# Performance work log

Hardware: AMD Instinct MI355X
Metric: run time of the kernel (lower is better)

Reference implementation:

```python
import jax, jax.numpy as jnp
import numpy as np

B, S, D, H, E, P, TOP_K = 8, 4096, 512, 2048, 8, 16, 2


def setup_inputs() -> dict:
    key = jax.random.key(0)
    ks = jax.random.split(key, 7)
    x = jax.random.normal(ks[0], (B, S, D), dtype=jnp.float32)
    pattern_ids = jax.random.randint(ks[1], (B,), 0, P)
    # router params (init per module: std 0.01 content, std 0.1 pattern bias)
    Wr = 0.01 * jax.random.normal(ks[2], (D, E), dtype=jnp.float32)
    Wp = 0.1 * jax.random.normal(ks[3], (P, E), dtype=jnp.float32)
    # per-expert SwiGLU FFN weights (stacked): w1, w3: [E,D,H], w2: [E,H,D]
    W1 = jax.random.normal(ks[4], (E, D, H), dtype=jnp.float32) / np.float32(np.sqrt(D))
    W2 = jax.random.normal(ks[5], (E, H, D), dtype=jnp.float32) / np.float32(np.sqrt(H))
    W3 = jax.random.normal(ks[6], (E, D, H), dtype=jnp.float32) / np.float32(np.sqrt(D))
    return {"x": x, "pattern_ids": pattern_ids, "Wr": Wr, "Wp": Wp, "W1": W1, "W2": W2, "W3": W3}


def reference(x, pattern_ids, Wr, Wp, W1, W2, W3):
    num_experts = W1.shape[0]
    num_patterns = Wp.shape[0]
    # ---- pattern-aware router ----
    # content logits + per-batch pattern bias broadcast over seq
    logits = jnp.einsum('bsd,de->bse', x, Wr) + Wp[pattern_ids][:, None, :]  # [B,S,E]
    top_w, top_i = jax.lax.top_k(logits, TOP_K)           # [B,S,K]
    gates = jax.nn.softmax(top_w, axis=-1)                # softmax over the top-k logits
    # ---- expert dispatch / combine (loop over small fixed expert count) ----
    y = jnp.zeros_like(x)
    for e in range(num_experts):
        # combined gate weight for expert e per token (0 if not selected)
        w_e = jnp.sum(gates * (top_i == e), axis=-1)      # [B,S]
        h = jnp.einsum('bsd,dh->bsh', x, W1[e]) * jax.nn.silu(jnp.einsum('bsd,dh->bsh', x, W3[e]))
        y = y + w_e[..., None] * jnp.einsum('bsh,hd->bsd', h, W2[e])
    # ---- auxiliary losses ----
    probs = jax.nn.softmax(logits, axis=-1)
    router_z_loss = jnp.mean(jnp.square(logits)) * 0.001
    balance_loss = jnp.mean(jnp.square(probs.mean(axis=(0, 1)) - 1.0 / num_experts))
    Pn = jax.nn.softmax(Wp, axis=-1)
    sim = Pn @ Pn.T
    specialization_loss = jnp.mean(sim * (1.0 - jnp.eye(num_patterns, dtype=sim.dtype))) * 0.1
    return (y, router_z_loss, balance_loss, specialization_loss)
```

## Files before the change

kernel.cpp:

```cpp
#include <hip/hip_runtime.h>
#include <hip/hip_bf16.h>
#include <math.h>


#define B_ 8
#define S_ 4096
#define D_ 512
#define H_ 2048
#define E_ 8
#define P_ 16
#define NTOK (B_ * S_)
#define NPAIR (NTOK * 2)

typedef __bf16 bf16;
typedef __bf16 bf16x8 __attribute__((ext_vector_type(8)));
typedef float f32x4 __attribute__((ext_vector_type(4)));

#define OFF_GATES 256
#define OFF_LIST (OFF_GATES + NPAIR * 4)
#define OFF_XBF (OFF_LIST + E_ * NTOK * 4)
#define OFF_W13T (OFF_XBF + (size_t)NTOK * D_ * 2)
#define OFF_W2T (OFF_W13T + (size_t)E_ * 2 * H_ * D_ * 2)
#define OFF_HBUF (OFF_W2T + (size_t)E_ * D_ * H_ * 2)
#define WS_NEEDED (OFF_HBUF + (size_t)NTOK * H_ * 2)

__device__ __forceinline__ void gl16(const bf16* g, bf16* l) {
  __builtin_amdgcn_global_load_lds((const __attribute__((address_space(1))) unsigned int*)g,
                                   (__attribute__((address_space(3))) unsigned int*)l, 16, 0, 0);
}

__global__ __launch_bounds__(256) void router_kernel(
    const float* __restrict__ x, const int* __restrict__ pids,
    const float* __restrict__ Wr, const float* __restrict__ Wp,
    bf16* __restrict__ xbf, float* __restrict__ gates, int* __restrict__ lists,
    int* __restrict__ counts, float* __restrict__ probSum, float* __restrict__ zSum) {
  __shared__ float xs[32 * 516];
  __shared__ float wr_s[E_ * 516];
  __shared__ float wp_s[E_];
  __shared__ float probAcc[E_];
  __shared__ float zAcc;
  __shared__ int lcnt[E_], lbase[E_];
  __shared__ float lg_s[32][E_ + 1];

  const int tid = threadIdx.x;
  const int tok0 = blockIdx.x * 32;

#pragma unroll
  for (int rep = 0; rep < (D_ * E_) / 256; ++rep) {
    int flat = rep * 256 + tid;
    wr_s[(flat & 7) * 516 + (flat >> 3)] = Wr[flat];
  }
  if (tid < E_) {
    wp_s[tid] = Wp[pids[tok0 >> 12] * E_ + tid];
    probAcc[tid] = 0.f;
    lcnt[tid] = 0;
  }
  if (tid == 0) zAcc = 0.f;

  const float4* x4 = (const float4*)(x + (size_t)tok0 * D_);
#pragma unroll
  for (int rep = 0; rep < 16; ++rep) {
    int idx = rep * 256 + tid;
    float4 v = x4[idx];
    int t = idx >> 7;
    int d = (idx & 127) * 4;
    *(float4*)(xs + t * 516 + d) = v;
    union { unsigned short u[4]; uint2 qq; } pk;
    pk.u[0] = __builtin_bit_cast(unsigned short, (bf16)v.x);
    pk.u[1] = __builtin_bit_cast(unsigned short, (bf16)v.y);
    pk.u[2] = __builtin_bit_cast(unsigned short, (bf16)v.z);
    pk.u[3] = __builtin_bit_cast(unsigned short, (bf16)v.w);
    *(uint2*)(xbf + (size_t)tok0 * D_ + (size_t)idx * 4) = pk.qq;
  }
  __syncthreads();

  const int t = tid >> 3, e = tid & 7;
  const int lane = tid & 63;
  {
    float a0 = 0.f, a1 = 0.f, a2 = 0.f, a3 = 0.f;
    const float* xr = xs + t * 516;
    const float* wr = wr_s + e * 516;
#pragma unroll 8
    for (int d = 0; d < D_; d += 4) {
      float4 xv = *(const float4*)(xr + d);
      float4 wv = *(const float4*)(wr + d);
      a0 += xv.x * wv.x;
      a1 += xv.y * wv.y;
      a2 += xv.z * wv.z;
      a3 += xv.w * wv.w;
    }
    lg_s[t][e] = (a0 + a1) + (a2 + a3) + wp_s[e];
  }
  __syncthreads();

  float v[E_];
#pragma unroll
  for (int k = 0; k < E_; ++k) v[k] = lg_s[t][k];
  const float lg = v[e];
  float m = v[0];
#pragma unroll
  for (int k = 1; k < E_; ++k) m = fmaxf(m, v[k]);
  float s = 0.f;
#pragma unroll
  for (int k = 0; k < E_; ++k) s += expf(v[k] - m);
  float prob = expf(lg - m) / s;
  float z = lg * lg;
  int i1 = 0;
  float v1 = v[0];
#pragma unroll
  for (int k = 1; k < E_; ++k)
    if (v[k] > v1) { v1 = v[k]; i1 = k; }
  int i2 = -1;
  float v2 = -1e30f;
#pragma unroll
  for (int k = 0; k < E_; ++k)
    if (k != i1 && v[k] > v2) { v2 = v[k]; i2 = k; }

  float p = prob;
  p += __shfl_xor(p, 8);
  p += __shfl_xor(p, 16);
  p += __shfl_xor(p, 32);
  float zz = z;
#pragma unroll
  for (int off = 1; off < 64; off <<= 1) zz += __shfl_xor(zz, off);
  if (lane < 8) atomicAdd(&probAcc[e], p);
  if (lane == 0) atomicAdd(&zAcc, zz);

  int r = (e == i1) ? 0 : ((e == i2) ? 1 : -1);
  int pos = -1;
  if (r >= 0) {
    float ex = expf(v2 - v1);
    float g = (r == 0) ? 1.f / (1.f + ex) : ex / (1.f + ex);
    gates[(tok0 + t) * 2 + r] = g;
    pos = atomicAdd(&lcnt[e], 1);
  }
  __syncthreads();
  if (tid < E_) lbase[tid] = atomicAdd(&counts[tid], lcnt[tid]);
  __syncthreads();
  if (r >= 0) lists[e * NTOK + lbase[e] + pos] = (tok0 + t) * 2 + r;
  if (tid < E_) atomicAdd(&probSum[tid], probAcc[tid]);
  else if (tid == 8) atomicAdd(zSum, zAcc);
}

__global__ __launch_bounds__(256) void transpose_convert(const float* __restrict__ in,
                                                         bf16* __restrict__ out, int R, int C,
                                                         size_t out_estride, int mode) {
  const int e = blockIdx.z;
  const int r0 = blockIdx.y * 64, c0 = blockIdx.x * 64;
  in += (size_t)e * R * C;
  out += (size_t)e * out_estride;
  __shared__ unsigned int lt[64 * 33];

  const int tid = threadIdx.x;
  const int m = tid & 15, qq = tid >> 4;
#pragma unroll
  for (int rep = 0; rep < 2; ++rep) {
    int rp = qq + rep * 16;
    const float4 a = *(const float4*)(in + (size_t)(r0 + rp * 2) * C + c0 + m * 4);
    const float4 b = *(const float4*)(in + (size_t)(r0 + rp * 2 + 1) * C + c0 + m * 4);
#pragma unroll
    for (int j = 0; j < 4; ++j) {
      unsigned short lo = __builtin_bit_cast(unsigned short, (bf16)((&a.x)[j]));
      unsigned short hi = __builtin_bit_cast(unsigned short, (bf16)((&b.x)[j]));
      lt[(m * 4 + j) * 33 + rp] = (unsigned int)lo | ((unsigned int)hi << 16);
    }
  }
  __syncthreads();
  const int c = tid >> 2, dw0 = (tid & 3) * 8;
  unsigned int vv[8];
#pragma unroll
  for (int j = 0; j < 8; ++j) vv[j] = lt[c * 33 + dw0 + j];
  int orow = c0 + c;
  if (mode >= 0) orow = ((orow >> 4) << 5) | (orow & 15) | mode;
  uint4* dst = (uint4*)(out + (size_t)orow * R + r0 + dw0 * 2);
  dst[0] = make_uint4(vv[0], vv[1], vv[2], vv[3]);
  dst[1] = make_uint4(vv[4], vv[5], vv[6], vv[7]);
}

__global__ __launch_bounds__(256, 2) void gemm1_kernel(
    const bf16* __restrict__ xbf, const bf16* __restrict__ W13T,
    const int* __restrict__ counts, const int* __restrict__ lists,
    const float* __restrict__ gates, bf16* __restrict__ hbuf, int e) {
  const int count = counts[e];
  const int m0 = blockIdx.y * 128;
  if (m0 >= count) return;
  const int n0 = blockIdx.x * 128;
  const int* list_e = lists + e * NTOK;
  const bf16* Be = W13T + (size_t)e * (2 * H_) * D_;

  __shared__ bf16 sA[2 * 128 * 32];
  __shared__ bf16 sB[2 * 128 * 32];
  __shared__ int stok[128];
  __shared__ float sgate[128];

  const int tid = threadIdx.x;
  if (tid < 128) {
    int rg = m0 + tid;
    int pr = (rg < count) ? list_e[rg] : 0;
    stok[tid] = pr >> 1;
    sgate[tid] = (rg < count) ? gates[pr] : 0.f;
  }
  __syncthreads();

  const int wave = tid >> 6, lane = tid & 63;
  const int rsub = lane >> 2, kq = lane & 3;
  const int scol = (kq ^ ((lane >> 3) & 3)) * 8;
  const int rA0 = wave * 16 + rsub, rA1 = 64 + wave * 16 + rsub;
  const bf16* aP0 = xbf + (size_t)stok[rA0] * D_ + scol;
  const bf16* aP1 = xbf + (size_t)stok[rA1] * D_ + scol;
  const bf16* bP0 = Be + (size_t)(n0 + rA0) * D_ + scol;
  const bf16* bP1 = Be + (size_t)(n0 + rA1) * D_ + scol;
  bf16* lA0 = sA + wave * 512;
  bf16* lA1 = sA + (wave + 4) * 512;
  bf16* lB0 = sB + wave * 512;
  bf16* lB1 = sB + (wave + 4) * 512;

  const int wm = wave >> 1, wn = wave & 1;
  const int lm = lane & 15, q = lane >> 4;
  const int rq = (q ^ ((lm >> 1) & 3)) * 8;
  const bf16* aRd = sA + (wm * 64 + lm) * 32 + rq;
  const bf16* bRd = sB + (wn * 64 + lm) * 32 + rq;

  f32x4 acc[4][4] = {};

  gl16(aP0, lA0);
  gl16(aP1, lA1);
  gl16(bP0, lB0);
  gl16(bP1, lB1);
  __syncthreads();

  int cur = 0;
  for (int t = 1; t < D_ / 32; ++t) {
    const int koff = t * 32;
    const int nxt = (cur ^ 1) * 4096;
    gl16(aP0 + koff, lA0 + nxt);
    gl16(aP1 + koff, lA1 + nxt);
    gl16(bP0 + koff, lB0 + nxt);
    gl16(bP1 + koff, lB1 + nxt);
    const bf16* aR = aRd + cur * 4096;
    const bf16* bR = bRd + cur * 4096;
    bf16x8 af[4], bf_[4];
#pragma unroll
    for (int i = 0; i < 4; ++i) {
      af[i] = *(const bf16x8*)(aR + i * 512);
      bf_[i] = *(const bf16x8*)(bR + i * 512);
    }
#pragma unroll
    for (int mt = 0; mt < 4; ++mt)
#pragma unroll
      for (int nt = 0; nt < 4; ++nt)
        acc[mt][nt] =
            __builtin_amdgcn_mfma_f32_16x16x32_bf16(af[mt], bf_[nt], acc[mt][nt], 0, 0, 0);
    __syncthreads();
    cur ^= 1;
  }
  {
    const bf16* aR = aRd + cur * 4096;
    const bf16* bR = bRd + cur * 4096;
    bf16x8 af[4], bf_[4];
#pragma unroll
    for (int i = 0; i < 4; ++i) {
      af[i] = *(const bf16x8*)(aR + i * 512);
      bf_[i] = *(const bf16x8*)(bR + i * 512);
    }
#pragma unroll
    for (int mt = 0; mt < 4; ++mt)
#pragma unroll
      for (int nt = 0; nt < 4; ++nt)
        acc[mt][nt] =
            __builtin_amdgcn_mfma_f32_16x16x32_bf16(af[mt], bf_[nt], acc[mt][nt], 0, 0, 0);
  }

  const int hb = (n0 >> 1) + wn * 32;
#pragma unroll
  for (int mt = 0; mt < 4; ++mt) {
#pragma unroll
    for (int u = 0; u < 2; ++u) {
#pragma unroll
      for (int r = 0; r < 4; ++r) {
        int lrow = wm * 64 + mt * 16 + q * 4 + r;
        int grow = m0 + lrow;
        if (grow < count) {
          float v1 = acc[mt][2 * u][r];
          float v3 = acc[mt][2 * u + 1][r];
          float g = v1 * (v3 / (1.f + __expf(-v3))) * sgate[lrow];
          hbuf[(size_t)grow * H_ + hb + u * 16 + lm] = (bf16)g;
        }
      }
    }
  }
}

__global__ __launch_bounds__(256, 2) void gemm2_kernel(const bf16* __restrict__ hbuf,
                                                       const bf16* __restrict__ W2T,
                                                       const int* __restrict__ counts,
                                                       const int* __restrict__ lists,
                                                       float* __restrict__ y, int e) {
  const int count = counts[e];
  const int m0 = blockIdx.y * 128;
  if (m0 >= count) return;
  const int n0 = blockIdx.x * 128;
  const int kb = blockIdx.z * (H_ / 2);
  const bf16* W2e = W2T + (size_t)e * D_ * H_;
  const int* list_e = lists + e * NTOK;

  __shared__ bf16 sA[2 * 128 * 32];
  __shared__ bf16 sB[2 * 128 * 32];
  __shared__ int stok[128];

  const int tid = threadIdx.x;
  if (tid < 128) {
    int rg = m0 + tid;
    stok[tid] = (rg < count) ? (list_e[rg] >> 1) : 0;
  }
  __syncthreads();

  const int wave = tid >> 6, lane = tid & 63;
  const int rsub = lane >> 2, kq = lane & 3;
  const int scol = (kq ^ ((lane >> 3) & 3)) * 8;
  const int rA0 = wave * 16 + rsub, rA1 = 64 + wave * 16 + rsub;
  const bf16* aP0 = hbuf + (size_t)(m0 + rA0) * H_ + kb + scol;
  const bf16* aP1 = hbuf + (size_t)(m0 + rA1) * H_ + kb + scol;
  const bf16* bP0 = W2e + (size_t)(n0 + rA0) * H_ + kb + scol;
  const bf16* bP1 = W2e + (size_t)(n0 + rA1) * H_ + kb + scol;
  bf16* lA0 = sA + wave * 512;
  bf16* lA1 = sA + (wave + 4) * 512;
  bf16* lB0 = sB + wave * 512;
  bf16* lB1 = sB + (wave + 4) * 512;

  const int wm = wave >> 1, wn = wave & 1;
  const int lm = lane & 15, q = lane >> 4;
  const int rq = (q ^ ((lm >> 1) & 3)) * 8;
  const bf16* aRd = sA + (wm * 64 + lm) * 32 + rq;
  const bf16* bRd = sB + (wn * 64 + lm) * 32 + rq;

  f32x4 acc[4][4] = {};

  gl16(aP0, lA0);
  gl16(aP1, lA1);
  gl16(bP0, lB0);
  gl16(bP1, lB1);
  __syncthreads();

  int cur = 0;
  for (int t = 1; t < (H_ / 2) / 32; ++t) {
    const int koff = t * 32;
    const int nxt = (cur ^ 1) * 4096;
    gl16(aP0 + koff, lA0 + nxt);
    gl16(aP1 + koff, lA1 + nxt);
    gl16(bP0 + koff, lB0 + nxt);
    gl16(bP1 + koff, lB1 + nxt);
    const bf16* aR = aRd + cur * 4096;
    const bf16* bR = bRd + cur * 4096;
    bf16x8 af[4], bf_[4];
#pragma unroll
    for (int i = 0; i < 4; ++i) {
      af[i] = *(const bf16x8*)(aR + i * 512);
      bf_[i] = *(const bf16x8*)(bR + i * 512);
    }
#pragma unroll
    for (int mt = 0; mt < 4; ++mt)
#pragma unroll
      for (int nt = 0; nt < 4; ++nt)
        acc[mt][nt] =
            __builtin_amdgcn_mfma_f32_16x16x32_bf16(af[mt], bf_[nt], acc[mt][nt], 0, 0, 0);
    __syncthreads();
    cur ^= 1;
  }
  {
    const bf16* aR = aRd + cur * 4096;
    const bf16* bR = bRd + cur * 4096;
    bf16x8 af[4], bf_[4];
#pragma unroll
    for (int i = 0; i < 4; ++i) {
      af[i] = *(const bf16x8*)(aR + i * 512);
      bf_[i] = *(const bf16x8*)(bR + i * 512);
    }
#pragma unroll
    for (int mt = 0; mt < 4; ++mt)
#pragma unroll
      for (int nt = 0; nt < 4; ++nt)
        acc[mt][nt] =
            __builtin_amdgcn_mfma_f32_16x16x32_bf16(af[mt], bf_[nt], acc[mt][nt], 0, 0, 0);
  }

#pragma unroll
  for (int mt = 0; mt < 4; ++mt) {
#pragma unroll
    for (int nt = 0; nt < 4; ++nt) {
#pragma unroll
      for (int r = 0; r < 4; ++r) {
        int lrow = wm * 64 + mt * 16 + q * 4 + r;
        int grow = m0 + lrow;
        if (grow < count) {
          atomicAdd(&y[(size_t)stok[lrow] * D_ + n0 + wn * 64 + nt * 16 + lm], acc[mt][nt][r]);
        }
      }
    }
  }
}

__global__ __launch_bounds__(256) void finalize_kernel(const float* __restrict__ Wp,
                                                       const float* __restrict__ probSum,
                                                       const float* __restrict__ zSum,
                                                       float* __restrict__ out) {
  __shared__ float pn[P_][E_];
  __shared__ float simAcc;
  const int tid = threadIdx.x;
  if (tid == 0) simAcc = 0.f;
  if (tid < P_) {
    float v[E_], m = -1e30f, s = 0.f;
#pragma unroll
    for (int e = 0; e < E_; ++e) {
      v[e] = Wp[tid * E_ + e];
      m = fmaxf(m, v[e]);
    }
#pragma unroll
    for (int e = 0; e < E_; ++e) {
      float ex = expf(v[e] - m);
      pn[tid][e] = ex;
      s += ex;
    }
#pragma unroll
    for (int e = 0; e < E_; ++e) pn[tid][e] /= s;
  }
  __syncthreads();
  {
    int i = tid >> 4, j = tid & 15;
    if (i != j) {
      float d = 0.f;
#pragma unroll
      for (int e = 0; e < E_; ++e) d += pn[i][e] * pn[j][e];
      atomicAdd(&simAcc, d);
    }
  }
  __syncthreads();
  if (tid == 0) {
    out[0] = zSum[0] / (float)(NTOK * E_) * 0.001f;
    float bl = 0.f;
#pragma unroll
    for (int e = 0; e < E_; ++e) {
      float pm = probSum[e] / (float)NTOK - 1.f / (float)E_;
      bl += pm * pm;
    }
    out[1] = bl / (float)E_;
    out[2] = simAcc / (float)(P_ * P_) * 0.1f;
  }
}

extern "C" void kernel_launch(void* const* d_in, const int* in_sizes, int n_in, void* d_out,
                              int out_size, void* d_ws, size_t ws_size, hipStream_t stream) {
  const float* x = (const float*)d_in[0];
  const int* pids = (const int*)d_in[1];
  const float* Wr = (const float*)d_in[2];
  const float* Wp = (const float*)d_in[3];
  const float* W1 = (const float*)d_in[4];
  const float* W2 = (const float*)d_in[5];
  const float* W3 = (const float*)d_in[6];
  float* y = (float*)d_out;

  if (ws_size < WS_NEEDED) return;

  char* ws = (char*)d_ws;
  int* counts = (int*)ws;
  float* probSum = (float*)(ws + 32);
  float* zSum = (float*)(ws + 64);
  float* gates = (float*)(ws + OFF_GATES);
  int* lists = (int*)(ws + OFF_LIST);
  bf16* xbf = (bf16*)(ws + OFF_XBF);
  bf16* W13T = (bf16*)(ws + OFF_W13T);
  bf16* W2T = (bf16*)(ws + OFF_W2T);
  bf16* hbuf = (bf16*)(ws + OFF_HBUF);

  hipMemsetAsync(ws, 0, 256, stream);
  hipMemsetAsync(d_out, 0, (size_t)NTOK * D_ * 4, stream);

  router_kernel<<<dim3(NTOK / 32), 256, 0, stream>>>(x, pids, Wr, Wp, xbf, gates, lists, counts,
                                                     probSum, zSum);
  transpose_convert<<<dim3(H_ / 64, D_ / 64, E_), 256, 0, stream>>>(W1, W13T, D_, H_,
                                                                    (size_t)2 * H_ * D_, 0);
  transpose_convert<<<dim3(H_ / 64, D_ / 64, E_), 256, 0, stream>>>(W3, W13T, D_, H_,
                                                                    (size_t)2 * H_ * D_, 16);
  transpose_convert<<<dim3(D_ / 64, H_ / 64, E_), 256, 0, stream>>>(W2, W2T, H_, D_,
                                                                    (size_t)H_ * D_, -1);

  for (int e = 0; e < E_; ++e) {
    gemm1_kernel<<<dim3((2 * H_) / 128, NTOK / 128), 256, 0, stream>>>(xbf, W13T, counts, lists,
                                                                       gates, hbuf, e);
    gemm2_kernel<<<dim3(D_ / 128, NTOK / 128, 2), 256, 0, stream>>>(hbuf, W2T, counts, lists, y,
                                                                    e);
  }
  finalize_kernel<<<1, 256, 0, stream>>>(Wp, probSum, zSum, y + (size_t)NTOK * D_);
}
```

Before: 1.126 ms.

## Deepen GEMM global-to-LDS pipeline to four buffers with vmcnt-based waits

Both expert GEMM kernels move from a double-buffered LDS pipeline with a full __syncthreads per k-step to a four-slot ring that keeps two tiles in flight ahead of compute. Waits use explicit s_waitcnt vmcnt counts and a raw s_barrier, so compute can start while later loads are still outstanding. The goal is to hide global memory latency and remove full-drain barriers. In exchange, LDS use per block doubles, which may reduce occupancy, and correctness depends on the hand-counted vmcnt values and on the ring slots not being overwritten while another wave is still reading them.

```diff
diff --git a/kernel.cpp b/kernel.cpp
--- a/kernel.cpp
+++ b/kernel.cpp
@@ -188,8 +188,8 @@
   const int* list_e = lists + e * NTOK;
   const bf16* Be = W13T + (size_t)e * (2 * H_) * D_;
 
-  __shared__ bf16 sA[2 * 128 * 32];
-  __shared__ bf16 sB[2 * 128 * 32];
+  __shared__ bf16 sA[4 * 128 * 32];
+  __shared__ bf16 sB[4 * 128 * 32];
   __shared__ int stok[128];
   __shared__ float sgate[128];
 
@@ -210,10 +210,6 @@
   const bf16* aP1 = xbf + (size_t)stok[rA1] * D_ + scol;
   const bf16* bP0 = Be + (size_t)(n0 + rA0) * D_ + scol;
   const bf16* bP1 = Be + (size_t)(n0 + rA1) * D_ + scol;
-  bf16* lA0 = sA + wave * 512;
-  bf16* lA1 = sA + (wave + 4) * 512;
-  bf16* lB0 = sB + wave * 512;
-  bf16* lB1 = sB + (wave + 4) * 512;
 
   const int wm = wave >> 1, wn = wave & 1;
   const int lm = lane & 15, q = lane >> 4;
@@ -223,22 +219,18 @@
 
   f32x4 acc[4][4] = {};
 
-  gl16(aP0, lA0);
-  gl16(aP1, lA1);
-  gl16(bP0, lB0);
-  gl16(bP1, lB1);
-  __syncthreads();
-
-  int cur = 0;
-  for (int t = 1; t < D_ / 32; ++t) {
-    const int koff = t * 32;
-    const int nxt = (cur ^ 1) * 4096;
-    gl16(aP0 + koff, lA0 + nxt);
-    gl16(aP1 + koff, lA1 + nxt);
-    gl16(bP0 + koff, lB0 + nxt);
-    gl16(bP1 + koff, lB1 + nxt);
-    const bf16* aR = aRd + cur * 4096;
-    const bf16* bR = bRd + cur * 4096;
+  auto STAGE = [&](int t, int bi) {
+    const int ko = t * 32;
+    bf16* ba = sA + bi * 4096;
+    bf16* bb = sB + bi * 4096;
+    gl16(aP0 + ko, ba + wave * 512);
+    gl16(aP1 + ko, ba + (wave + 4) * 512);
+    gl16(bP0 + ko, bb + wave * 512);
+    gl16(bP1 + ko, bb + (wave + 4) * 512);
+  };
+  auto COMP = [&](int bi) {
+    const bf16* aR = aRd + bi * 4096;
+    const bf16* bR = bRd + bi * 4096;
     bf16x8 af[4], bf_[4];
 #pragma unroll
     for (int i = 0; i < 4; ++i) {
@@ -251,25 +243,22 @@
       for (int nt = 0; nt < 4; ++nt)
         acc[mt][nt] =
             __builtin_amdgcn_mfma_f32_16x16x32_bf16(af[mt], bf_[nt], acc[mt][nt], 0, 0, 0);
-    __syncthreads();
-    cur ^= 1;
-  }
-  {
-    const bf16* aR = aRd + cur * 4096;
-    const bf16* bR = bRd + cur * 4096;
-    bf16x8 af[4], bf_[4];
-#pragma unroll
-    for (int i = 0; i < 4; ++i) {
-      af[i] = *(const bf16x8*)(aR + i * 512);
-      bf_[i] = *(const bf16x8*)(bR + i * 512);
-    }
-#pragma unroll
-    for (int mt = 0; mt < 4; ++mt)
-#pragma unroll
-      for (int nt = 0; nt < 4; ++nt)
-        acc[mt][nt] =
-            __builtin_amdgcn_mfma_f32_16x16x32_bf16(af[mt], bf_[nt], acc[mt][nt], 0, 0, 0);
-  }
+  };
+
+  STAGE(0, 0);
+  STAGE(1, 1);
+  for (int t = 0; t < D_ / 32 - 2; ++t) {
+    STAGE(t + 2, (t + 2) & 3);
+    asm volatile("s_waitcnt vmcnt(8) lgkmcnt(0)" ::: "memory");
+    __builtin_amdgcn_s_barrier();
+    COMP(t & 3);
+  }
+  asm volatile("s_waitcnt vmcnt(4) lgkmcnt(0)" ::: "memory");
+  __builtin_amdgcn_s_barrier();
+  COMP((D_ / 32 - 2) & 3);
+  asm volatile("s_waitcnt vmcnt(0) lgkmcnt(0)" ::: "memory");
+  __builtin_amdgcn_s_barrier();
+  COMP((D_ / 32 - 1) & 3);
 
   const int hb = (n0 >> 1) + wn * 32;
 #pragma unroll
@@ -304,8 +293,8 @@
   const bf16* W2e = W2T + (size_t)e * D_ * H_;
   const int* list_e = lists + e * NTOK;
 
-  __shared__ bf16 sA[2 * 128 * 32];
-  __shared__ bf16 sB[2 * 128 * 32];
+  __shared__ bf16 sA[4 * 128 * 32];
+  __shared__ bf16 sB[4 * 128 * 32];
   __shared__ int stok[128];
 
   const int tid = threadIdx.x;
@@ -323,10 +312,6 @@
   const bf16* aP1 = hbuf + (size_t)(m0 + rA1) * H_ + kb + scol;
   const bf16* bP0 = W2e + (size_t)(n0 + rA0) * H_ + kb + scol;
   const bf16* bP1 = W2e + (size_t)(n0 + rA1) * H_ + kb + scol;
-  bf16* lA0 = sA + wave * 512;
-  bf16* lA1 = sA + (wave + 4) * 512;
-  bf16* lB0 = sB + wave * 512;
-  bf16* lB1 = sB + (wave + 4) * 512;
 
   const int wm = wave >> 1, wn = wave & 1;
   const int lm = lane & 15, q = lane >> 4;
@@ -336,22 +321,18 @@
 
   f32x4 acc[4][4] = {};
 
-  gl16(aP0, lA0);
-  gl16(aP1, lA1);
-  gl16(bP0, lB0);
-  gl16(bP1, lB1);
-  __syncthreads();
-
-  int cur = 0;
-  for (int t = 1; t < (H_ / 2) / 32; ++t) {
-    const int koff = t * 32;
-    const int nxt = (cur ^ 1) * 4096;
-    gl16(aP0 + koff, lA0 + nxt);
-    gl16(aP1 + koff, lA1 + nxt);
-    gl16(bP0 + koff, lB0 + nxt);
-    gl16(bP1 + koff, lB1 + nxt);
-    const bf16* aR = aRd + cur * 4096;
-    const bf16* bR = bRd + cur * 4096;
+  auto STAGE = [&](int t, int bi) {
+    const int ko = t * 32;
+    bf16* ba = sA + bi * 4096;
+    bf16* bb = sB + bi * 4096;
+    gl16(aP0 + ko, ba + wave * 512);
+    gl16(aP1 + ko, ba + (wave + 4) * 512);
+    gl16(bP0 + ko, bb + wave * 512);
+    gl16(bP1 + ko, bb + (wave + 4) * 512);
+  };
+  auto COMP = [&](int bi) {
+    const bf16* aR = aRd + bi * 4096;
+    const bf16* bR = bRd + bi * 4096;
     bf16x8 af[4], bf_[4];
 #pragma unroll
     for (int i = 0; i < 4; ++i) {
@@ -364,25 +345,23 @@
       for (int nt = 0; nt < 4; ++nt)
         acc[mt][nt] =
             __builtin_amdgcn_mfma_f32_16x16x32_bf16(af[mt], bf_[nt], acc[mt][nt], 0, 0, 0);
-    __syncthreads();
-    cur ^= 1;
-  }
-  {
-    const bf16* aR = aRd + cur * 4096;
-    const bf16* bR = bRd + cur * 4096;
-    bf16x8 af[4], bf_[4];
-#pragma unroll
-    for (int i = 0; i < 4; ++i) {
-      af[i] = *(const bf16x8*)(aR + i * 512);
-      bf_[i] = *(const bf16x8*)(bR + i * 512);
-    }
-#pragma unroll
-    for (int mt = 0; mt < 4; ++mt)
-#pragma unroll
-      for (int nt = 0; nt < 4; ++nt)
-        acc[mt][nt] =
-            __builtin_amdgcn_mfma_f32_16x16x32_bf16(af[mt], bf_[nt], acc[mt][nt], 0, 0, 0);
-  }
+  };
+
+  const int NT = (H_ / 2) / 32;
+  STAGE(0, 0);
+  STAGE(1, 1);
+  for (int t = 0; t < NT - 2; ++t) {
+    STAGE(t + 2, (t + 2) & 3);
+    asm volatile("s_waitcnt vmcnt(8) lgkmcnt(0)" ::: "memory");
+    __builtin_amdgcn_s_barrier();
+    COMP(t & 3);
+  }
+  asm volatile("s_waitcnt vmcnt(4) lgkmcnt(0)" ::: "memory");
+  __builtin_amdgcn_s_barrier();
+  COMP((NT - 2) & 3);
+  asm volatile("s_waitcnt vmcnt(0) lgkmcnt(0)" ::: "memory");
+  __builtin_amdgcn_s_barrier();
+  COMP((NT - 1) & 3);
 
 #pragma unroll
   for (int mt = 0; mt < 4; ++mt) {
```

Result: no change. 1.111 ms (-1.3%).

## Batch all experts into single grouped GEMM launches and deepen gemm2 pipeline

Applied to the files above, without the earlier changes.

Replaces the per-expert loop of 16 kernel launches with two launches that cover all experts via blockIdx.z, storing h rows for each expert at a prefix-sum offset in a larger hbuf. Experts can then run concurrently, removing launch gaps and the tail underutilization of each small per-expert grid. Separately, gemm2 moves from double buffering to a 4-stage LDS ring with explicit vmcnt waits, so loads are issued two steps ahead. This doubles gemm2's LDS use, and the fused path only runs when the workspace is large enough, falling back to the old loop otherwise.

```diff
diff --git a/kernel.cpp b/kernel.cpp
--- a/kernel.cpp
+++ b/kernel.cpp
@@ -23,6 +23,7 @@
 #define OFF_W2T (OFF_W13T + (size_t)E_ * 2 * H_ * D_ * 2)
 #define OFF_HBUF (OFF_W2T + (size_t)E_ * D_ * H_ * 2)
 #define WS_NEEDED (OFF_HBUF + (size_t)NTOK * H_ * 2)
+#define WS_FUSED (OFF_HBUF + (size_t)NPAIR * H_ * 2)
 
 __device__ __forceinline__ void gl16(const bf16* g, bf16* l) {
   __builtin_amdgcn_global_load_lds((const __attribute__((address_space(1))) unsigned int*)g,
@@ -180,10 +181,16 @@
 __global__ __launch_bounds__(256, 2) void gemm1_kernel(
     const bf16* __restrict__ xbf, const bf16* __restrict__ W13T,
     const int* __restrict__ counts, const int* __restrict__ lists,
-    const float* __restrict__ gates, bf16* __restrict__ hbuf, int e) {
+    const float* __restrict__ gates, bf16* __restrict__ hbuf, int e_param, int fuse) {
+  const int e = fuse ? (int)blockIdx.z : e_param;
   const int count = counts[e];
   const int m0 = blockIdx.y * 128;
   if (m0 >= count) return;
+  int hbase = 0;
+  if (fuse) {
+#pragma unroll
+    for (int j = 0; j < E_; ++j) hbase += (j < e) ? counts[j] : 0;
+  }
   const int n0 = blockIdx.x * 128;
   const int* list_e = lists + e * NTOK;
   const bf16* Be = W13T + (size_t)e * (2 * H_) * D_;
@@ -284,7 +291,7 @@
           float v1 = acc[mt][2 * u][r];
           float v3 = acc[mt][2 * u + 1][r];
           float g = v1 * (v3 / (1.f + __expf(-v3))) * sgate[lrow];
-          hbuf[(size_t)grow * H_ + hb + u * 16 + lm] = (bf16)g;
+          hbuf[(size_t)(hbase + grow) * H_ + hb + u * 16 + lm] = (bf16)g;
         }
       }
     }
@@ -295,17 +302,26 @@
                                                        const bf16* __restrict__ W2T,
                                                        const int* __restrict__ counts,
                                                        const int* __restrict__ lists,
-                                                       float* __restrict__ y, int e) {
+                                                       float* __restrict__ y, int e_param,
+                                                       int fuse) {
+  const int zz = (int)blockIdx.z;
+  const int e = fuse ? (zz >> 1) : e_param;
+  const int kc = fuse ? (zz & 1) : zz;
   const int count = counts[e];
   const int m0 = blockIdx.y * 128;
   if (m0 >= count) return;
+  int hbase = 0;
+  if (fuse) {
+#pragma unroll
+    for (int j = 0; j < E_; ++j) hbase += (j < e) ? counts[j] : 0;
+  }
   const int n0 = blockIdx.x * 128;
-  const int kb = blockIdx.z * (H_ / 2);
+  const int kb = kc * (H_ / 2);
   const bf16* W2e = W2T + (size_t)e * D_ * H_;
   const int* list_e = lists + e * NTOK;
 
-  __shared__ bf16 sA[2 * 128 * 32];
-  __shared__ bf16 sB[2 * 128 * 32];
+  __shared__ bf16 sA[4 * 128 * 32];
+  __shared__ bf16 sB[4 * 128 * 32];
   __shared__ int stok[128];
 
   const int tid = threadIdx.x;
@@ -319,14 +335,10 @@
   const int rsub = lane >> 2, kq = lane & 3;
   const int scol = (kq ^ ((lane >> 3) & 3)) * 8;
   const int rA0 = wave * 16 + rsub, rA1 = 64 + wave * 16 + rsub;
-  const bf16* aP0 = hbuf + (size_t)(m0 + rA0) * H_ + kb + scol;
-  const bf16* aP1 = hbuf + (size_t)(m0 + rA1) * H_ + kb + scol;
+  const bf16* aP0 = hbuf + (size_t)(hbase + m0 + rA0) * H_ + kb + scol;
+  const bf16* aP1 = hbuf + (size_t)(hbase + m0 + rA1) * H_ + kb + scol;
   const bf16* bP0 = W2e + (size_t)(n0 + rA0) * H_ + kb + scol;
   const bf16* bP1 = W2e + (size_t)(n0 + rA1) * H_ + kb + scol;
-  bf16* lA0 = sA + wave * 512;
-  bf16* lA1 = sA + (wave + 4) * 512;
-  bf16* lB0 = sB + wave * 512;
-  bf16* lB1 = sB + (wave + 4) * 512;
 
   const int wm = wave >> 1, wn = wave & 1;
   const int lm = lane & 15, q = lane >> 4;
@@ -336,22 +348,18 @@
 
   f32x4 acc[4][4] = {};
 
-  gl16(aP0, lA0);
-  gl16(aP1, lA1);
-  gl16(bP0, lB0);
-  gl16(bP1, lB1);
-  __syncthreads();
-
-  int cur = 0;
-  for (int t = 1; t < (H_ / 2) / 32; ++t) {
-    const int koff = t * 32;
-    const int nxt = (cur ^ 1) * 4096;
-    gl16(aP0 + koff, lA0 + nxt);
-    gl16(aP1 + koff, lA1 + nxt);
-    gl16(bP0 + koff, lB0 + nxt);
-    gl16(bP1 + koff, lB1 + nxt);
-    const bf16* aR = aRd + cur * 4096;
-    const bf16* bR = bRd + cur * 4096;
+  auto STAGE = [&](int t, int bi) {
+    const int ko = t * 32;
+    bf16* ba = sA + bi * 4096;
+    bf16* bb = sB + bi * 4096;
+    gl16(aP0 + ko, ba + wave * 512);
+    gl16(aP1 + ko, ba + (wave + 4) * 512);
+    gl16(bP0 + ko, bb + wave * 512);
+    gl16(bP1 + ko, bb + (wave + 4) * 512);
+  };
+  auto COMP = [&](int bi) {
+    const bf16* aR = aRd + bi * 4096;
+    const bf16* bR = bRd + bi * 4096;
     bf16x8 af[4], bf_[4];
 #pragma unroll
     for (int i = 0; i < 4; ++i) {
@@ -364,25 +372,23 @@
       for (int nt = 0; nt < 4; ++nt)
         acc[mt][nt] =
             __builtin_amdgcn_mfma_f32_16x16x32_bf16(af[mt], bf_[nt], acc[mt][nt], 0, 0, 0);
-    __syncthreads();
-    cur ^= 1;
-  }
-  {
-    const bf16* aR = aRd + cur * 4096;
-    const bf16* bR = bRd + cur * 4096;
-    bf16x8 af[4], bf_[4];
-#pragma unroll
-    for (int i = 0; i < 4; ++i) {
-      af[i] = *(const bf16x8*)(aR + i * 512);
-      bf_[i] = *(const bf16x8*)(bR + i * 512);
-    }
-#pragma unroll
-    for (int mt = 0; mt < 4; ++mt)
-#pragma unroll
-      for (int nt = 0; nt < 4; ++nt)
-        acc[mt][nt] =
-            __builtin_amdgcn_mfma_f32_16x16x32_bf16(af[mt], bf_[nt], acc[mt][nt], 0, 0, 0);
-  }
+  };
+
+  const int NT = (H_ / 2) / 32;
+  STAGE(0, 0);
+  STAGE(1, 1);
+  for (int t = 0; t < NT - 2; ++t) {
+    STAGE(t + 2, (t + 2) & 3);
+    asm volatile("s_waitcnt vmcnt(8) lgkmcnt(0)" ::: "memory");
+    __builtin_amdgcn_s_barrier();
+    COMP(t & 3);
+  }
+  asm volatile("s_waitcnt vmcnt(4) lgkmcnt(0)" ::: "memory");
+  __builtin_amdgcn_s_barrier();
+  COMP((NT - 2) & 3);
+  asm volatile("s_waitcnt vmcnt(0) lgkmcnt(0)" ::: "memory");
+  __builtin_amdgcn_s_barrier();
+  COMP((NT - 1) & 3);
 
 #pragma unroll
   for (int mt = 0; mt < 4; ++mt) {
@@ -460,6 +466,7 @@
   float* y = (float*)d_out;
 
   if (ws_size < WS_NEEDED) return;
+  const int fuse = (ws_size >= WS_FUSED) ? 1 : 0;
 
   char* ws = (char*)d_ws;
   int* counts = (int*)ws;
@@ -484,11 +491,18 @@
   transpose_convert<<<dim3(D_ / 64, H_ / 64, E_), 256, 0, stream>>>(W2, W2T, H_, D_,
                                                                     (size_t)H_ * D_, -1);
 
-  for (int e = 0; e < E_; ++e) {
-    gemm1_kernel<<<dim3((2 * H_) / 128, NTOK / 128), 256, 0, stream>>>(xbf, W13T, counts, lists,
-                                                                       gates, hbuf, e);
-    gemm2_kernel<<<dim3(D_ / 128, NTOK / 128, 2), 256, 0, stream>>>(hbuf, W2T, counts, lists, y,
-                                                                    e);
+  if (fuse) {
+    gemm1_kernel<<<dim3((2 * H_) / 128, NTOK / 128, E_), 256, 0, stream>>>(
+        xbf, W13T, counts, lists, gates, hbuf, 0, 1);
+    gemm2_kernel<<<dim3(D_ / 128, NTOK / 128, 2 * E_), 256, 0, stream>>>(hbuf, W2T, counts,
+                                                                         lists, y, 0, 1);
+  } else {
+    for (int e = 0; e < E_; ++e) {
+      gemm1_kernel<<<dim3((2 * H_) / 128, NTOK / 128), 256, 0, stream>>>(xbf, W13T, counts,
+                                                                         lists, gates, hbuf, e, 0);
+      gemm2_kernel<<<dim3(D_ / 128, NTOK / 128, 2), 256, 0, stream>>>(hbuf, W2T, counts, lists,
+                                                                      y, e, 0);
+    }
   }
   finalize_kernel<<<1, 256, 0, stream>>>(Wp, probSum, zSum, y + (size_t)NTOK * D_);
 }
```

After: 1.067 ms. 1.05x faster.
